# Kernel tuning notes

Hardware: AMD Instinct MI355X
Metric: run time of the kernel (lower is better)

The kernel has to match this reference:

```python
import jax, jax.numpy as jnp
import numpy as np

DIM = 1024
NHEADS = 16
HEAD_DIM = DIM // NHEADS
SCALE = HEAD_DIM ** -0.5
B, N = 4, 2048


def setup_inputs() -> dict:
    key = jax.random.key(0)
    ks = jax.random.split(key, 11)
    s = 1.0 / np.sqrt(DIM)
    inp = {
        "query": jax.random.normal(ks[0], (B, N, DIM), jnp.float32),
        "key": jax.random.normal(ks[1], (B, N, DIM), jnp.float32),
        "value": jax.random.normal(ks[2], (B, N, DIM), jnp.float32),
        "Wq": jax.random.normal(ks[3], (DIM, DIM), jnp.float32) * s,
        "bq": jnp.zeros((DIM,), jnp.float32),
        "Wk": jax.random.normal(ks[4], (DIM, DIM), jnp.float32) * s,
        "bk": jnp.zeros((DIM,), jnp.float32),
        "Wv": jax.random.normal(ks[5], (DIM, DIM), jnp.float32) * s,
        "bv": jnp.zeros((DIM,), jnp.float32),
        "Wo": jax.random.normal(ks[6], (DIM, DIM), jnp.float32) * s,
        "bo": jnp.zeros((DIM,), jnp.float32),
    }
    return inp


def reference(query, key, value, Wq, bq, Wk, bk, Wv, bv, Wo, bo):
    b, n, c = query.shape
    # linear projections (torch Linear: x @ W.T + b)
    q = query @ Wq.T + bq
    k = key @ Wk.T + bk
    v = value @ Wv.T + bv
    # 'b n (h d) -> (b h) n d'
    def split_heads(t):
        return t.reshape(b, -1, NHEADS, HEAD_DIM).transpose(0, 2, 1, 3).reshape(b * NHEADS, -1, HEAD_DIM)
    q, k, v = split_heads(q), split_heads(k), split_heads(v)
    attn = jax.nn.softmax(jnp.einsum('bnd,bmd->bnm', q, k) * SCALE, axis=-1)
    # faithful to original: raw reshape [(b h), n, d] -> [b, n, c] (no head transpose back)
    x = jnp.einsum('bnm,bmd->bnd', attn, v).reshape(b, n, c)
    x = x @ Wo.T + bo
    return x
```

## Files before the change

### kernel.cpp

```cpp
#include <hip/hip_runtime.h>
#include <cstdint>
#include <cstddef>

#define NHEADS 16
#define HD 64
#define SEQ 2048
#define BATCH 4
#define DIMSZ 1024
#define MR (BATCH * SEQ)

typedef __attribute__((ext_vector_type(8))) short short8;
typedef __attribute__((ext_vector_type(4))) short short4v;
typedef __attribute__((ext_vector_type(4))) float f32x4;

typedef __attribute__((address_space(1))) const unsigned int as1_u32;
typedef __attribute__((address_space(3))) unsigned int as3_u32;

__device__ __forceinline__ unsigned short f2bf(float x) {
  union { float f; unsigned int u; } v; v.f = x;
  unsigned int r = v.u + 0x7FFFu + ((v.u >> 16) & 1u);
  return (unsigned short)(r >> 16);
}

__device__ __forceinline__ f32x4 mfma16(short8 a, short8 b, f32x4 c) {
  return __builtin_amdgcn_mfma_f32_16x16x32_bf16(a, b, c, 0, 0, 0);
}

__device__ __forceinline__ void gload_lds16(const void* g, void* l) {
  __builtin_amdgcn_global_load_lds((as1_u32*)g, (as3_u32*)l, 16, 0, 0);
}

__device__ __forceinline__ int swzfn(int r) { return ((r ^ (r >> 3)) & 7) << 4; }

struct Cvt7 {
  const float* s[7];
  unsigned short* d[7];
  int n4[7];
};

__global__ __launch_bounds__(256) void cvt7_k(Cvt7 a) {
  const int t = blockIdx.y;
  const float4* s = (const float4*)a.s[t];
  ushort4* d = (ushort4*)a.d[t];
  const int n4 = a.n4[t];
  for (int i = blockIdx.x * 256 + threadIdx.x; i < n4; i += gridDim.x * 256) {
    float4 f = s[i];
    ushort4 u;
    u.x = f2bf(f.x); u.y = f2bf(f.y); u.z = f2bf(f.z); u.w = f2bf(f.w);
    d[i] = u;
  }
}

struct GemmArgs {
  const unsigned short* A[3];
  const unsigned short* Bt[3];
  const float* bias[3];
  unsigned short* Cb[3];
  float* Cf[3];
  float scale[3];
  int vt[3];
};

template <bool BF16OUT>
__global__ __launch_bounds__(256) void gemm_bt_k(GemmArgs g) {
  const int z = blockIdx.z;
  const unsigned short* __restrict__ A = g.A[z];
  const unsigned short* __restrict__ Bt = g.Bt[z];
  const float* __restrict__ bias = g.bias[z];

  __shared__ unsigned short As[128 * 32];
  __shared__ unsigned short Bs[128 * 32];

  const int tid = threadIdx.x;
  const int lane = tid & 63;
  const int wave = tid >> 6;
  const int bm = blockIdx.x * 128;
  const int bn = blockIdx.y * 128;
  const int wm = (wave >> 1) * 64;
  const int wn = (wave & 1) * 64;

  const int srow = wave * 16 + (lane >> 2);
  const int scol = (lane & 3) * 8;
  const unsigned short* a_src = A + (size_t)(bm + srow) * DIMSZ + scol;
  const unsigned short* b_src = Bt + (size_t)(bn + srow) * DIMSZ + scol;
  char* a_dst = (char*)As + (size_t)(wave * 16) * 64;
  char* b_dst = (char*)Bs + (size_t)(wave * 16) * 64;

  const int fr = lane & 15;
  const int fk = (lane >> 4) * 8;

  f32x4 acc[4][4];
#pragma unroll
  for (int m = 0; m < 4; m++)
#pragma unroll
    for (int n = 0; n < 4; n++) acc[m][n] = (f32x4){0.f, 0.f, 0.f, 0.f};

  for (int k0 = 0; k0 < DIMSZ; k0 += 32) {
    __syncthreads();
    gload_lds16(a_src + k0, a_dst);
    gload_lds16(a_src + (size_t)64 * DIMSZ + k0, a_dst + 64 * 64);
    gload_lds16(b_src + k0, b_dst);
    gload_lds16(b_src + (size_t)64 * DIMSZ + k0, b_dst + 64 * 64);
    __syncthreads();

    short8 af[4], bfr[4];
#pragma unroll
    for (int m = 0; m < 4; m++) af[m] = *(const short8*)&As[(wm + m * 16 + fr) * 32 + fk];
#pragma unroll
    for (int n = 0; n < 4; n++) bfr[n] = *(const short8*)&Bs[(wn + n * 16 + fr) * 32 + fk];
#pragma unroll
    for (int m = 0; m < 4; m++)
#pragma unroll
      for (int n = 0; n < 4; n++) acc[m][n] = mfma16(af[m], bfr[n], acc[m][n]);
  }

  const int r4 = (lane >> 4) * 4;
  const float sc = g.scale[z];
  if (g.vt[z]) {
    unsigned short* vtp = g.Cb[z];
#pragma unroll
    for (int n = 0; n < 4; n++) {
      const int c = bn + wn + n * 16 + fr;
      const float bv = bias[c];
#pragma unroll
      for (int m = 0; m < 4; m++) {
        const int rr = bm + wm + m * 16 + r4;
        ushort4 u;
        u.x = f2bf((acc[m][n][0] + bv) * sc);
        u.y = f2bf((acc[m][n][1] + bv) * sc);
        u.z = f2bf((acc[m][n][2] + bv) * sc);
        u.w = f2bf((acc[m][n][3] + bv) * sc);
        const size_t idx =
            ((size_t)((rr >> 11) * NHEADS + (c >> 6)) * HD + (c & 63)) * SEQ + (rr & (SEQ - 1));
        *(ushort4*)&vtp[idx] = u;
      }
    }
  } else {
#pragma unroll
    for (int n = 0; n < 4; n++) {
      const int c = bn + wn + n * 16 + fr;
      const float bv = bias[c];
#pragma unroll
      for (int m = 0; m < 4; m++) {
#pragma unroll
        for (int j = 0; j < 4; j++) {
          const int r = bm + wm + m * 16 + r4 + j;
          const float val = (acc[m][n][j] + bv) * sc;
          if (BF16OUT)
            g.Cb[z][(size_t)r * DIMSZ + c] = f2bf(val);
          else
            g.Cf[z][(size_t)r * DIMSZ + c] = val;
        }
      }
    }
  }
}

__global__ __launch_bounds__(512) void attn_k(const unsigned short* __restrict__ q,
                                              const unsigned short* __restrict__ k,
                                              const unsigned short* __restrict__ vt,
                                              unsigned short* __restrict__ o) {
  const int tid = threadIdx.x;
  const int lane = tid & 63;
  const int wave = tid >> 6;
  const int bh = blockIdx.y;
  const int b = bh >> 4;
  const int h = bh & 15;
  const int q0 = blockIdx.x * 128;

  __shared__ unsigned short Ks[2][64 * 64];
  __shared__ unsigned short Vs[2][64 * 64];

  const int fr = lane & 15;
  const int g4 = lane >> 4;
  const int fkb = g4 * 16;

  const size_t qrow = (size_t)b * SEQ + q0 + wave * 16 + fr;
  const unsigned short* qp = q + qrow * DIMSZ + h * HD + g4 * 8;
  const short8 qa0 = *(const short8*)(qp);
  const short8 qa1 = *(const short8*)(qp + 32);

  float m_run = -1e30f, l_run = 0.f;
  f32x4 oacc[4];
#pragma unroll
  for (int n = 0; n < 4; n++) oacc[n] = (f32x4){0.f, 0.f, 0.f, 0.f};

  int koff[4][2];
  int voff[4][4];
#pragma unroll
  for (int n = 0; n < 4; n++) {
    const int row = fr + 16 * n;
    const int swz = swzfn(row);
    koff[n][0] = (row * 128 + fkb) ^ swz;
    koff[n][1] = (row * 128 + 64 + fkb) ^ swz;
#pragma unroll
    for (int c = 0; c < 4; c++) voff[n][c] = (row * 128 + (c * 32 + 8 * g4)) ^ swz;
  }

  const int klrow = lane >> 3;
  const int kcb = (lane & 7) * 16;
  const int srow = wave * 8 + klrow;
  const int scol = (kcb ^ swzfn(srow)) >> 1;
  const unsigned short* ksrc =
      k + (size_t)b * SEQ * DIMSZ + h * HD + (size_t)srow * DIMSZ + scol;
  const unsigned short* vsrc =
      vt + (size_t)bh * HD * SEQ + (size_t)srow * SEQ + scol;

  auto stage = [&](int t, int buf) {
    const size_t kv0 = (size_t)t * 64;
    gload_lds16(ksrc + kv0 * DIMSZ, (char*)Ks[buf] + wave * 1024);
    gload_lds16(vsrc + kv0, (char*)Vs[buf] + wave * 1024);
  };

  stage(0, 0);
  __syncthreads();
  int cur = 0;

  for (int t = 0; t < SEQ / 64; ++t) {
    if (t + 1 < SEQ / 64) stage(t + 1, cur ^ 1);

    const char* Kc = (const char*)Ks[cur];
    const char* Vc = (const char*)Vs[cur];

    f32x4 s[4];
#pragma unroll
    for (int n = 0; n < 4; n++) {
      const short8 kb0 = *(const short8*)(Kc + koff[n][0]);
      const short8 kb1 = *(const short8*)(Kc + koff[n][1]);
      f32x4 tacc = (f32x4){0.f, 0.f, 0.f, 0.f};
      tacc = mfma16(kb0, qa0, tacc);
      tacc = mfma16(kb1, qa1, tacc);
      s[n] = tacc;
    }

    float pm = -1e30f;
#pragma unroll
    for (int n = 0; n < 4; n++)
#pragma unroll
      for (int jj = 0; jj < 4; jj++) pm = fmaxf(pm, s[n][jj]);
    pm = fmaxf(pm, __shfl_xor(pm, 16));
    pm = fmaxf(pm, __shfl_xor(pm, 32));
    const float mn = fmaxf(m_run, pm);
    const float sf = __expf(m_run - mn);
    m_run = mn;

    unsigned pu[4][2];
    float rs = 0.f;
#pragma unroll
    for (int n = 0; n < 4; n++) {
      const float p0 = __expf(s[n][0] - mn);
      const float p1 = __expf(s[n][1] - mn);
      const float p2 = __expf(s[n][2] - mn);
      const float p3 = __expf(s[n][3] - mn);
      rs += (p0 + p1) + (p2 + p3);
      pu[n][0] = (unsigned)f2bf(p0) | ((unsigned)f2bf(p1) << 16);
      pu[n][1] = (unsigned)f2bf(p2) | ((unsigned)f2bf(p3) << 16);
    }
    l_run = l_run * sf + rs;

    float sfr[4];
#pragma unroll
    for (int jj = 0; jj < 4; jj++) sfr[jj] = __shfl(sf, 20 * g4 + jj);
#pragma unroll
    for (int n = 0; n < 4; n++)
#pragma unroll
      for (int jj = 0; jj < 4; jj++) oacc[n][jj] *= sfr[jj];

    union { unsigned u[4]; short8 v; } pa0, pa1;
    pa0.u[0] = pu[0][0]; pa0.u[1] = pu[0][1]; pa0.u[2] = pu[1][0]; pa0.u[3] = pu[1][1];
    pa1.u[0] = pu[2][0]; pa1.u[1] = pu[2][1]; pa1.u[2] = pu[3][0]; pa1.u[3] = pu[3][1];

#pragma unroll
    for (int n = 0; n < 4; n++) {
      union { short4v h[2]; short8 v; } vb0, vb1;
      vb0.h[0] = *(const short4v*)(Vc + voff[n][0]);
      vb0.h[1] = *(const short4v*)(Vc + voff[n][1]);
      vb1.h[0] = *(const short4v*)(Vc + voff[n][2]);
      vb1.h[1] = *(const short4v*)(Vc + voff[n][3]);
      oacc[n] = mfma16(pa0.v, vb0.v, oacc[n]);
      oacc[n] = mfma16(pa1.v, vb1.v, oacc[n]);
    }

    __syncthreads();
    cur ^= 1;
  }

  l_run += __shfl_xor(l_run, 16);
  l_run += __shfl_xor(l_run, 32);
  float inv[4];
#pragma unroll
  for (int jj = 0; jj < 4; jj++) inv[jj] = 1.f / __shfl(l_run, 20 * g4 + jj);
#pragma unroll
  for (int n = 0; n < 4; n++)
#pragma unroll
    for (int jj = 0; jj < 4; jj++) {
      const int row = q0 + wave * 16 + 4 * g4 + jj;
      o[((size_t)bh * SEQ + row) * HD + fr + 16 * n] = f2bf(oacc[n][jj] * inv[jj]);
    }
}

extern "C" void kernel_launch(void* const* d_in, const int* in_sizes, int n_in,
                              void* d_out, int out_size, void* d_ws, size_t ws_size,
                              hipStream_t stream) {
  (void)in_sizes; (void)n_in; (void)out_size; (void)ws_size;
  const float* query = (const float*)d_in[0];
  const float* key_i = (const float*)d_in[1];
  const float* value = (const float*)d_in[2];
  const float* Wq = (const float*)d_in[3];
  const float* bq = (const float*)d_in[4];
  const float* Wk = (const float*)d_in[5];
  const float* bk = (const float*)d_in[6];
  const float* Wv = (const float*)d_in[7];
  const float* bv = (const float*)d_in[8];
  const float* Wo = (const float*)d_in[9];
  const float* bo = (const float*)d_in[10];
  float* out = (float*)d_out;

  char* ws = (char*)d_ws;
  size_t off = 0;
  auto alloc = [&](size_t bytes) -> char* {
    char* p = ws + off;
    off += (bytes + 255) & ~(size_t)255;
    return p;
  };
  const size_t big = (size_t)MR * DIMSZ * 2;
  const size_t wsz = (size_t)DIMSZ * DIMSZ * 2;
  unsigned short* xq = (unsigned short*)alloc(big);
  unsigned short* xk = (unsigned short*)alloc(big);
  unsigned short* xv = (unsigned short*)alloc(big);
  unsigned short* wqb = (unsigned short*)alloc(wsz);
  unsigned short* wkb = (unsigned short*)alloc(wsz);
  unsigned short* wvb = (unsigned short*)alloc(wsz);
  unsigned short* wob = (unsigned short*)alloc(wsz);
  unsigned short* qb = (unsigned short*)alloc(big);
  unsigned short* kb = (unsigned short*)alloc(big);
  unsigned short* vtb = (unsigned short*)alloc(big);
  unsigned short* ob = xq;

  Cvt7 ca;
  ca.s[0] = query; ca.d[0] = xq; ca.n4[0] = MR * DIMSZ / 4;
  ca.s[1] = key_i; ca.d[1] = xk; ca.n4[1] = MR * DIMSZ / 4;
  ca.s[2] = value; ca.d[2] = xv; ca.n4[2] = MR * DIMSZ / 4;
  ca.s[3] = Wq;    ca.d[3] = wqb; ca.n4[3] = DIMSZ * DIMSZ / 4;
  ca.s[4] = Wk;    ca.d[4] = wkb; ca.n4[4] = DIMSZ * DIMSZ / 4;
  ca.s[5] = Wv;    ca.d[5] = wvb; ca.n4[5] = DIMSZ * DIMSZ / 4;
  ca.s[6] = Wo;    ca.d[6] = wob; ca.n4[6] = DIMSZ * DIMSZ / 4;
  cvt7_k<<<dim3(1024, 7), 256, 0, stream>>>(ca);

  GemmArgs gp;
  gp.A[0] = xq; gp.A[1] = xk; gp.A[2] = xv;
  gp.Bt[0] = wqb; gp.Bt[1] = wkb; gp.Bt[2] = wvb;
  gp.bias[0] = bq; gp.bias[1] = bk; gp.bias[2] = bv;
  gp.Cb[0] = qb; gp.Cb[1] = kb; gp.Cb[2] = vtb;
  gp.Cf[0] = nullptr; gp.Cf[1] = nullptr; gp.Cf[2] = nullptr;
  gp.scale[0] = 0.125f; gp.scale[1] = 1.f; gp.scale[2] = 1.f;
  gp.vt[0] = 0; gp.vt[1] = 0; gp.vt[2] = 1;
  gemm_bt_k<true><<<dim3(MR / 128, DIMSZ / 128, 3), 256, 0, stream>>>(gp);

  attn_k<<<dim3(SEQ / 128, BATCH * NHEADS), 512, 0, stream>>>(qb, kb, vtb, ob);

  GemmArgs go;
  go.A[0] = ob; go.A[1] = ob; go.A[2] = ob;
  go.Bt[0] = wob; go.Bt[1] = wob; go.Bt[2] = wob;
  go.bias[0] = bo; go.bias[1] = bo; go.bias[2] = bo;
  go.Cb[0] = nullptr; go.Cb[1] = nullptr; go.Cb[2] = nullptr;
  go.Cf[0] = out; go.Cf[1] = out; go.Cf[2] = out;
  go.scale[0] = 1.f; go.scale[1] = 1.f; go.scale[2] = 1.f;
  go.vt[0] = 0; go.vt[1] = 0; go.vt[2] = 0;
  gemm_bt_k<false><<<dim3(MR / 128, DIMSZ / 128, 1), 256, 0, stream>>>(go);
}
```

Measured before the change: 391.9 us.

## Double-buffer GEMM LDS tiles and use lazy-rescale exp2 softmax in attention

```diff
diff --git a/kernel.cpp b/kernel.cpp
--- a/kernel.cpp
+++ b/kernel.cpp
@@ -68,8 +68,8 @@
   const unsigned short* __restrict__ Bt = g.Bt[z];
   const float* __restrict__ bias = g.bias[z];
 
-  __shared__ unsigned short As[128 * 32];
-  __shared__ unsigned short Bs[128 * 32];
+  __shared__ unsigned short As[2][128 * 32];
+  __shared__ unsigned short Bs[2][128 * 32];
 
   const int tid = threadIdx.x;
   const int lane = tid & 63;
@@ -83,8 +83,7 @@
   const int scol = (lane & 3) * 8;
   const unsigned short* a_src = A + (size_t)(bm + srow) * DIMSZ + scol;
   const unsigned short* b_src = Bt + (size_t)(bn + srow) * DIMSZ + scol;
-  char* a_dst = (char*)As + (size_t)(wave * 16) * 64;
-  char* b_dst = (char*)Bs + (size_t)(wave * 16) * 64;
+  const int dstoff = wave * 16 * 64;
 
   const int fr = lane & 15;
   const int fk = (lane >> 4) * 8;
@@ -95,23 +94,34 @@
 #pragma unroll
     for (int n = 0; n < 4; n++) acc[m][n] = (f32x4){0.f, 0.f, 0.f, 0.f};
 
+  auto stageg = [&](int k0, int buf) {
+    gload_lds16(a_src + k0, (char*)As[buf] + dstoff);
+    gload_lds16(a_src + (size_t)64 * DIMSZ + k0, (char*)As[buf] + dstoff + 64 * 64);
+    gload_lds16(b_src + k0, (char*)Bs[buf] + dstoff);
+    gload_lds16(b_src + (size_t)64 * DIMSZ + k0, (char*)Bs[buf] + dstoff + 64 * 64);
+  };
+
+  stageg(0, 0);
+  __syncthreads();
+  int cur = 0;
+
   for (int k0 = 0; k0 < DIMSZ; k0 += 32) {
+    if (k0 + 32 < DIMSZ) stageg(k0 + 32, cur ^ 1);
+
+    const unsigned short* Ac = As[cur];
+    const unsigned short* Bc = Bs[cur];
+    short8 af[4], bfr[4];
+#pragma unroll
+    for (int m = 0; m < 4; m++) af[m] = *(const short8*)&Ac[(wm + m * 16 + fr) * 32 + fk];
+#pragma unroll
+    for (int n = 0; n < 4; n++) bfr[n] = *(const short8*)&Bc[(wn + n * 16 + fr) * 32 + fk];
+#pragma unroll
+    for (int m = 0; m < 4; m++)
+#pragma unroll
+      for (int n = 0; n < 4; n++) acc[m][n] = mfma16(af[m], bfr[n], acc[m][n]);
+
     __syncthreads();
-    gload_lds16(a_src + k0, a_dst);
-    gload_lds16(a_src + (size_t)64 * DIMSZ + k0, a_dst + 64 * 64);
-    gload_lds16(b_src + k0, b_dst);
-    gload_lds16(b_src + (size_t)64 * DIMSZ + k0, b_dst + 64 * 64);
-    __syncthreads();
-
-    short8 af[4], bfr[4];
-#pragma unroll
-    for (int m = 0; m < 4; m++) af[m] = *(const short8*)&As[(wm + m * 16 + fr) * 32 + fk];
-#pragma unroll
-    for (int n = 0; n < 4; n++) bfr[n] = *(const short8*)&Bs[(wn + n * 16 + fr) * 32 + fk];
-#pragma unroll
-    for (int m = 0; m < 4; m++)
-#pragma unroll
-      for (int n = 0; n < 4; n++) acc[m][n] = mfma16(af[m], bfr[n], acc[m][n]);
+    cur ^= 1;
   }
 
   const int r4 = (lane >> 4) * 4;
@@ -240,31 +250,33 @@
       for (int jj = 0; jj < 4; jj++) pm = fmaxf(pm, s[n][jj]);
     pm = fmaxf(pm, __shfl_xor(pm, 16));
     pm = fmaxf(pm, __shfl_xor(pm, 32));
-    const float mn = fmaxf(m_run, pm);
-    const float sf = __expf(m_run - mn);
-    m_run = mn;
+    if (__any(pm > m_run + 11.0f)) {
+      const float mn = fmaxf(m_run, pm);
+      const float sf = exp2f(m_run - mn);
+      m_run = mn;
+      l_run *= sf;
+      float sfr[4];
+#pragma unroll
+      for (int jj = 0; jj < 4; jj++) sfr[jj] = __shfl(sf, 20 * g4 + jj);
+#pragma unroll
+      for (int n = 0; n < 4; n++)
+#pragma unroll
+        for (int jj = 0; jj < 4; jj++) oacc[n][jj] *= sfr[jj];
+    }
 
     unsigned pu[4][2];
     float rs = 0.f;
 #pragma unroll
     for (int n = 0; n < 4; n++) {
-      const float p0 = __expf(s[n][0] - mn);
-      const float p1 = __expf(s[n][1] - mn);
-      const float p2 = __expf(s[n][2] - mn);
-      const float p3 = __expf(s[n][3] - mn);
+      const float p0 = exp2f(s[n][0] - m_run);
+      const float p1 = exp2f(s[n][1] - m_run);
+      const float p2 = exp2f(s[n][2] - m_run);
+      const float p3 = exp2f(s[n][3] - m_run);
       rs += (p0 + p1) + (p2 + p3);
       pu[n][0] = (unsigned)f2bf(p0) | ((unsigned)f2bf(p1) << 16);
       pu[n][1] = (unsigned)f2bf(p2) | ((unsigned)f2bf(p3) << 16);
     }
-    l_run = l_run * sf + rs;
-
-    float sfr[4];
-#pragma unroll
-    for (int jj = 0; jj < 4; jj++) sfr[jj] = __shfl(sf, 20 * g4 + jj);
-#pragma unroll
-    for (int n = 0; n < 4; n++)
-#pragma unroll
-      for (int jj = 0; jj < 4; jj++) oacc[n][jj] *= sfr[jj];
+    l_run += rs;
 
     union { unsigned u[4]; short8 v; } pa0, pa1;
     pa0.u[0] = pu[0][0]; pa0.u[1] = pu[0][1]; pa0.u[2] = pu[1][0]; pa0.u[3] = pu[1][1];
@@ -353,7 +365,7 @@
   gp.bias[0] = bq; gp.bias[1] = bk; gp.bias[2] = bv;
   gp.Cb[0] = qb; gp.Cb[1] = kb; gp.Cb[2] = vtb;
   gp.Cf[0] = nullptr; gp.Cf[1] = nullptr; gp.Cf[2] = nullptr;
-  gp.scale[0] = 0.125f; gp.scale[1] = 1.f; gp.scale[2] = 1.f;
+  gp.scale[0] = 0.125f * 1.44269504f; gp.scale[1] = 1.f; gp.scale[2] = 1.f;
   gp.vt[0] = 0; gp.vt[1] = 0; gp.vt[2] = 1;
   gemm_bt_k<true><<<dim3(MR / 128, DIMSZ / 128, 3), 256, 0, stream>>>(gp);
 
```

Result: slower. 431.2 us (+10.0%).
